# Kernel tuning notes

Hardware: AMD Instinct MI355X
Metric: run time of the kernel (lower is better)

The kernel has to match this reference:

```python
import jax, jax.numpy as jnp
import numpy as np

VOCAB, POS_V, NER_V, DEPREL_V = 50000, 50, 10, 40
EMB, POS_D, NER_D, MEM = 300, 30, 30, 200
NUM_LAYERS = 2


def setup_inputs() -> dict:
    key = jax.random.key(0)
    ks = jax.random.split(key, 12)
    B, L = 32, 100
    adj = jax.random.randint(ks[0], (B, L, L), 0, DEPREL_V)
    words = jax.random.randint(ks[1], (B, L), 0, VOCAB)
    pos = jax.random.randint(ks[2], (B, L), 0, POS_V)
    ner = jax.random.randint(ks[3], (B, L), 0, NER_V)
    s = 0.02
    emb = jax.random.normal(ks[4], (VOCAB, EMB), jnp.float32) * s
    pos_emb = jax.random.normal(ks[5], (POS_V, POS_D), jnp.float32) * s
    ner_emb = jax.random.normal(ks[6], (NER_V, NER_D), jnp.float32) * s
    deprel_emb = jax.random.normal(ks[7], (DEPREL_V, MEM), jnp.float32) * s
    deprel_emb = deprel_emb.at[0].set(0.0)  # padding_idx=0
    in_dim = EMB + POS_D + NER_D
    Wp = jax.random.normal(ks[8], (MEM, in_dim), jnp.float32) * s
    bp = jnp.zeros((MEM,), jnp.float32)
    W0 = jax.random.normal(ks[9], (MEM, MEM), jnp.float32) * s
    b0 = jnp.zeros((MEM,), jnp.float32)
    W1 = jax.random.normal(ks[10], (MEM, MEM), jnp.float32) * s
    b1 = jnp.zeros((MEM,), jnp.float32)
    return {"adj": adj, "words": words, "pos": pos, "ner": ner,
            "emb": emb, "pos_emb": pos_emb, "ner_emb": ner_emb,
            "deprel_emb": deprel_emb, "Wp": Wp, "bp": bp,
            "W0": W0, "b0": b0, "W1": W1, "b1": b1}


def reference(adj, words, pos, ner, emb, pos_emb, ner_emb, deprel_emb,
              Wp, bp, W0, b0, W1, b1):
    # embedding lookups + concat  -> [B, L, in_dim]
    embs = jnp.concatenate([emb[words], pos_emb[pos], ner_emb[ner]], axis=-1)
    # preprocessor linear (diagonal_deprel branch)  -> [B, L, D]
    x = embs @ Wp.T + bp
    # per-edge relation embedding gather  -> [B, L, L, D]
    deprel_adj = deprel_emb[adj]
    adj_m = (adj != 0).astype(jnp.float32)            # [B, L, L]
    denom = adj_m.sum(2)[..., None] + 1.0             # [B, L, 1]
    mask = ((adj_m.sum(2) + adj_m.sum(1)) == 0)[..., None]  # [B, L, 1]
    for W, b in ((W0, b0), (W1, b1)):
        # diagonal deprel aggregation: (deprel_adj * x[:,None]) summed over neighbors
        Ax = jnp.einsum('blmd,bmd->bld', deprel_adj, x)
        AxW = (Ax @ W.T + b) + (x @ W.T + b)
        x = jax.nn.relu(AxW / denom)
    return x, mask
```

## Files before the change

kernel.cpp:

```cpp
#include <hip/hip_runtime.h>
#include <hip/hip_bf16.h>

#define BB 32
#define LL 100
#define DD 200
#define KIN 360
#define NP (BB*LL)
#define RNUM 40
#define LT 13
#define NT 8

__device__ __forceinline__ void fma4(float4& a, const float4& w, float s) {
    a.x = fmaf(w.x, s, a.x);
    a.y = fmaf(w.y, s, a.y);
    a.z = fmaf(w.z, s, a.z);
    a.w = fmaf(w.w, s, a.w);
}
__device__ __forceinline__ unsigned bf16rn(float f) {
    unsigned u = __float_as_uint(f);
    return (u + 0x7fffu + ((u >> 16) & 1u)) >> 16;
}
__device__ __forceinline__ unsigned pk2(float a, float b) {
    return bf16rn(a) | (bf16rn(b) << 16);
}
__device__ __forceinline__ float lo16(unsigned u) { return __uint_as_float(u << 16); }
__device__ __forceinline__ float hi16(unsigned u) { return __uint_as_float(u & 0xffff0000u); }

__global__ __launch_bounds__(256) void prep_transpose_kernel(
        const int* __restrict__ adj,
        const float* __restrict__ Wp, const float* __restrict__ W0, const float* __restrict__ W1,
        float* __restrict__ WpT, float* __restrict__ W0T, float* __restrict__ W1T,
        float* __restrict__ invd, float* __restrict__ mask_out) {
    int bid = blockIdx.x, tid = threadIdx.x;
    if (bid < 25) {
        int t = bid * 256 + tid;
        int half = t & 1;
        int pl = t >> 1;
        int b = pl / LL, l = pl % LL;
        const int4* row = (const int4*)(adj + (size_t)pl * LL);
        int q0 = half ? 13 : 0, q1 = half ? 25 : 13;
        int rc = 0;
        for (int i = q0; i < q1; ++i) {
            int4 a = row[i];
            rc += (a.x != 0) + (a.y != 0) + (a.z != 0) + (a.w != 0);
        }
        const int* base = adj + (size_t)b * LL * LL + l;
        int cc = 0;
        for (int m = half * 50; m < half * 50 + 50; ++m) cc += (base[(size_t)m * LL] != 0);
        rc += __shfl_xor(rc, 1);
        cc += __shfl_xor(cc, 1);
        if (!half) {
            invd[pl] = 1.0f / (float)(rc + 1);
            mask_out[pl] = (rc + cc == 0) ? 1.0f : 0.0f;
        }
    } else {
        int i = (bid - 25) * 256 + tid;
        if (i < 18000) {
            int k = i / 50, o = (i % 50) * 4;
            float4 v;
            v.x = Wp[(size_t)(o + 0) * KIN + k];
            v.y = Wp[(size_t)(o + 1) * KIN + k];
            v.z = Wp[(size_t)(o + 2) * KIN + k];
            v.w = Wp[(size_t)(o + 3) * KIN + k];
            ((float4*)WpT)[i] = v;
        } else if (i < 28000) {
            int q = i - 18000;
            int k = q / 50, o = (q % 50) * 4;
            float4 v;
            v.x = W0[(size_t)(o + 0) * DD + k];
            v.y = W0[(size_t)(o + 1) * DD + k];
            v.z = W0[(size_t)(o + 2) * DD + k];
            v.w = W0[(size_t)(o + 3) * DD + k];
            ((float4*)W0T)[q] = v;
        } else if (i < 38000) {
            int q = i - 28000;
            int k = q / 50, o = (q % 50) * 4;
            float4 v;
            v.x = W1[(size_t)(o + 0) * DD + k];
            v.y = W1[(size_t)(o + 1) * DD + k];
            v.z = W1[(size_t)(o + 2) * DD + k];
            v.w = W1[(size_t)(o + 3) * DD + k];
            ((float4*)W1T)[q] = v;
        }
    }
}

__global__ __launch_bounds__(512, 4) void embed_gemv_kernel(
        const int* __restrict__ words, const int* __restrict__ pos, const int* __restrict__ ner,
        const float* __restrict__ emb, const float* __restrict__ pose, const float* __restrict__ nere,
        const float* __restrict__ wpt, const float* __restrict__ bp,
        float* __restrict__ xA) {
    __shared__ float es[8 * KIN];
    __shared__ float4 red[8 * 8 * 50];
    int tid = threadIdx.x;
    int pbase = blockIdx.x * 8;

    float2* es2 = (float2*)es;
    for (int idx = tid; idx < 8 * 180; idx += 512) {
        int p = idx / 180, j2 = idx % 180;
        int gp = pbase + p;
        float2 v;
        if (j2 < 150)      v = ((const float2*)emb)[(size_t)words[gp] * 150 + j2];
        else if (j2 < 165) v = ((const float2*)pose)[pos[gp] * 15 + (j2 - 150)];
        else               v = ((const float2*)nere)[ner[gp] * 15 + (j2 - 165)];
        es2[idx] = v;
    }
    __syncthreads();

    int lane = tid & 63, w = tid >> 6;
    bool act = lane < 50;
    int oq = act ? lane : 49;
    int kq0 = (w < 5) ? 12 * w : 60 + 10 * (w - 5);
    int npair = (w < 5) ? 6 : 5;
    int kqlast = kq0 + 2 * npair - 1;
    const float4* wt4 = (const float4*)wpt;
    const float4* es4 = (const float4*)es;

    float4 a[8];
    #pragma unroll
    for (int p = 0; p < 8; ++p) a[p] = make_float4(0.f, 0.f, 0.f, 0.f);

    float4 wc[8], wn[8];
    #pragma unroll
    for (int q = 0; q < 2; ++q)
        #pragma unroll
        for (int j = 0; j < 4; ++j)
            wc[q * 4 + j] = wt4[(size_t)(4 * (kq0 + q) + j) * 50 + oq];

    for (int pr = 0; pr < npair; ++pr) {
        int nb = kq0 + 2 * pr + 2;
        int nbA = nb <= kqlast ? nb : kq0;
        int nbB = nb + 1 <= kqlast ? nb + 1 : kq0;
        #pragma unroll
        for (int j = 0; j < 4; ++j) wn[j]     = wt4[(size_t)(4 * nbA + j) * 50 + oq];
        #pragma unroll
        for (int j = 0; j < 4; ++j) wn[4 + j] = wt4[(size_t)(4 * nbB + j) * 50 + oq];
        #pragma unroll
        for (int q = 0; q < 2; ++q) {
            int kq = kq0 + 2 * pr + q;
            #pragma unroll
            for (int p = 0; p < 8; ++p) {
                float4 s = es4[p * 90 + kq];
                fma4(a[p], wc[q * 4 + 0], s.x); fma4(a[p], wc[q * 4 + 1], s.y);
                fma4(a[p], wc[q * 4 + 2], s.z); fma4(a[p], wc[q * 4 + 3], s.w);
            }
        }
        #pragma unroll
        for (int j = 0; j < 8; ++j) wc[j] = wn[j];
    }

    if (act) {
        #pragma unroll
        for (int p = 0; p < 8; ++p) red[w * 400 + p * 50 + oq] = a[p];
    }
    __syncthreads();
    for (int t = tid; t < 400; t += 512) {
        int oq2 = t % 50;
        float4 v = ((const float4*)bp)[oq2];
        #pragma unroll
        for (int s = 0; s < 8; ++s) {
            float4 r = red[s * 400 + t];
            v.x += r.x; v.y += r.y; v.z += r.z; v.w += r.w;
        }
        ((float4*)xA)[(size_t)(pbase + t / 50) * 50 + oq2] = v;
    }
}

__global__ __launch_bounds__(1024, 4) void layer_kernel(
        const float* __restrict__ x, const int* __restrict__ adj,
        const float* __restrict__ deprel, const float* __restrict__ wt,
        const float* __restrict__ bias, const float* __restrict__ invd,
        float* __restrict__ out) {
    __shared__ alignas(16) char smem[58912];
    uint2* deps_b = (uint2*)smem;
    unsigned* adjp = (unsigned*)(smem + 16000);
    float4* Sh = (float4*)(smem + 17312);
    float4* Sfin = (float4*)smem;

    int b = blockIdx.y, tile = blockIdx.x;
    int l0 = tile * LT;
    int lcnt = min(LT, LL - l0);
    int tid = threadIdx.x;
    const float4* x4 = (const float4*)x;

    for (int i = tid; i < RNUM * 50; i += 1024) {
        float4 v = ((const float4*)deprel)[i];
        deps_b[i] = make_uint2(pk2(v.x, v.y), pk2(v.z, v.w));
    }
    for (int i = tid; i < lcnt * 25; i += 1024) {
        int li = i / 25, mg = i % 25;
        int4 a = ((const int4*)(adj + (size_t)(b * LL + l0 + li) * LL))[mg];
        adjp[i] = (unsigned)a.x | ((unsigned)a.y << 8) | ((unsigned)a.z << 16) | ((unsigned)a.w << 24);
    }
    __syncthreads();

    int lane = tid & 63, w = tid >> 6;
    int lg = w & 3, sq = w >> 2;
    bool act = lane < 50;
    int dq = lane;

    float4 acc[4];
    #pragma unroll
    for (int i = 0; i < 4; ++i) acc[i] = make_float4(0.f, 0.f, 0.f, 0.f);
    if (act) {
        int mg0 = (sq == 0) ? 0 : 1 + 6 * sq;
        int mg1 = mg0 + ((sq == 0) ? 7 : 6);
        float4 xc[4], xn[4];
        #pragma unroll
        for (int mm = 0; mm < 4; ++mm)
            xc[mm] = x4[(size_t)(b * LL + 4 * mg0 + mm) * 50 + dq];
        for (int mg = mg0; mg < mg1; ++mg) {
            int mgn = (mg + 1 < mg1) ? mg + 1 : mg;
            #pragma unroll
            for (int mm = 0; mm < 4; ++mm)
                xn[mm] = x4[(size_t)(b * LL + 4 * mgn + mm) * 50 + dq];
            unsigned ap[4];
            #pragma unroll
            for (int i = 0; i < 4; ++i) {
                int li = lg + 4 * i;
                ap[i] = (li < lcnt) ? adjp[li * 25 + mg] : 0u;
            }
            #pragma unroll
            for (int mm = 0; mm < 4; ++mm) {
                #pragma unroll
                for (int i = 0; i < 4; ++i) {
                    unsigned r = (ap[i] >> (8 * mm)) & 0xffu;
                    uint2 dv = deps_b[r * 50 + dq];
                    acc[i].x = fmaf(lo16(dv.x), xc[mm].x, acc[i].x);
                    acc[i].y = fmaf(hi16(dv.x), xc[mm].y, acc[i].y);
                    acc[i].z = fmaf(lo16(dv.y), xc[mm].z, acc[i].z);
                    acc[i].w = fmaf(hi16(dv.y), xc[mm].w, acc[i].w);
                }
            }
            #pragma unroll
            for (int mm = 0; mm < 4; ++mm) xc[mm] = xn[mm];
        }
        #pragma unroll
        for (int i = 0; i < 4; ++i) {
            int li = lg + 4 * i;
            if (li < lcnt) Sh[sq * 650 + li * 50 + dq] = acc[i];
        }
    }
    __syncthreads();

    for (int t2 = tid; t2 < 650; t2 += 1024) {
        int li = t2 / 50;
        if (li < lcnt) {
            float4 s0 = Sh[t2], s1 = Sh[650 + t2], s2 = Sh[1300 + t2], s3 = Sh[1950 + t2];
            float4 xr = x4[(size_t)(b * LL + l0 + li) * 50 + (t2 % 50)];
            float4 s;
            s.x = s0.x + s1.x + s2.x + s3.x + xr.x;
            s.y = s0.y + s1.y + s2.y + s3.y + xr.y;
            s.z = s0.z + s1.z + s2.z + s3.z + xr.z;
            s.w = s0.w + s1.w + s2.w + s3.w + xr.w;
            Sfin[t2] = s;
        }
    }
    __syncthreads();

    const float4* wt4 = (const float4*)wt;
    int oq = act ? lane : 49;
    int kq0 = (sq < 2) ? 13 * sq : 26 + 12 * (sq - 2);
    int kcnt = (sq < 2) ? 13 : 12;
    int npair = kcnt >> 1;
    int kqlast = kq0 + kcnt - 1;
    float4 ba[4];
    #pragma unroll
    for (int i = 0; i < 4; ++i) ba[i] = make_float4(0.f, 0.f, 0.f, 0.f);

    float4 wc[8], wn[8];
    #pragma unroll
    for (int q = 0; q < 2; ++q)
        #pragma unroll
        for (int j = 0; j < 4; ++j)
            wc[q * 4 + j] = wt4[(size_t)(4 * (kq0 + q) + j) * 50 + oq];

    int lic[4];
    #pragma unroll
    for (int i = 0; i < 4; ++i) {
        int li = lg + 4 * i;
        lic[i] = li < lcnt ? li : lcnt - 1;
    }

    for (int pr = 0; pr < npair; ++pr) {
        int nb = kq0 + 2 * pr + 2;
        int nbA = nb <= kqlast ? nb : kq0;
        int nbB = nb + 1 <= kqlast ? nb + 1 : kq0;
        #pragma unroll
        for (int j = 0; j < 4; ++j) wn[j]     = wt4[(size_t)(4 * nbA + j) * 50 + oq];
        #pragma unroll
        for (int j = 0; j < 4; ++j) wn[4 + j] = wt4[(size_t)(4 * nbB + j) * 50 + oq];
        #pragma unroll
        for (int q = 0; q < 2; ++q) {
            int kq = kq0 + 2 * pr + q;
            #pragma unroll
            for (int i = 0; i < 4; ++i) {
                float4 s = Sfin[lic[i] * 50 + kq];
                fma4(ba[i], wc[q * 4 + 0], s.x); fma4(ba[i], wc[q * 4 + 1], s.y);
                fma4(ba[i], wc[q * 4 + 2], s.z); fma4(ba[i], wc[q * 4 + 3], s.w);
            }
        }
        #pragma unroll
        for (int j = 0; j < 8; ++j) wc[j] = wn[j];
    }
    if (kcnt & 1) {
        #pragma unroll
        for (int i = 0; i < 4; ++i) {
            float4 s = Sfin[lic[i] * 50 + kqlast];
            fma4(ba[i], wc[0], s.x); fma4(ba[i], wc[1], s.y);
            fma4(ba[i], wc[2], s.z); fma4(ba[i], wc[3], s.w);
        }
    }

    if (act) {
        #pragma unroll
        for (int i = 0; i < 4; ++i) {
            int li = lg + 4 * i;
            if (li < lcnt) Sh[sq * 650 + li * 50 + oq] = ba[i];
        }
    }
    __syncthreads();

    for (int t2 = tid; t2 < 650; t2 += 1024) {
        int li = t2 / 50, oq2 = t2 % 50;
        if (li < lcnt) {
            float4 v0 = Sh[t2], v1 = Sh[650 + t2], v2 = Sh[1300 + t2], v3 = Sh[1950 + t2];
            float4 bb = ((const float4*)bias)[oq2];
            int p = b * LL + l0 + li;
            float sc = invd[p];
            float4 v;
            v.x = fmaxf((v0.x + v1.x + v2.x + v3.x + 2.f * bb.x) * sc, 0.f);
            v.y = fmaxf((v0.y + v1.y + v2.y + v3.y + 2.f * bb.y) * sc, 0.f);
            v.z = fmaxf((v0.z + v1.z + v2.z + v3.z + 2.f * bb.z) * sc, 0.f);
            v.w = fmaxf((v0.w + v1.w + v2.w + v3.w + 2.f * bb.w) * sc, 0.f);
            ((float4*)out)[(size_t)p * 50 + oq2] = v;
        }
    }
}

extern "C" void kernel_launch(void* const* d_in, const int* in_sizes, int n_in,
                              void* d_out, int out_size, void* d_ws, size_t ws_size,
                              hipStream_t stream) {
    const int*   adj   = (const int*)d_in[0];
    const int*   words = (const int*)d_in[1];
    const int*   pos   = (const int*)d_in[2];
    const int*   ner   = (const int*)d_in[3];
    const float* emb   = (const float*)d_in[4];
    const float* pose  = (const float*)d_in[5];
    const float* nere  = (const float*)d_in[6];
    const float* dep   = (const float*)d_in[7];
    const float* Wp    = (const float*)d_in[8];
    const float* bp    = (const float*)d_in[9];
    const float* W0    = (const float*)d_in[10];
    const float* b0    = (const float*)d_in[11];
    const float* W1    = (const float*)d_in[12];
    const float* b1    = (const float*)d_in[13];
    float* out = (float*)d_out;
    float* ws  = (float*)d_ws;

    float* xA   = ws;
    float* xB   = ws + 640000;
    float* WpT  = ws + 1280000;
    float* W0T  = ws + 1352000;
    float* W1T  = ws + 1392000;
    float* invd = ws + 1432000;

    prep_transpose_kernel<<<25 + 149, 256, 0, stream>>>(adj, Wp, W0, W1, WpT, W0T, W1T,
                                                        invd, out + (size_t)NP * DD);
    embed_gemv_kernel<<<NP / 8, 512, 0, stream>>>(words, pos, ner, emb, pose, nere,
                                                  WpT, bp, xA);
    layer_kernel<<<dim3(NT, BB), 1024, 0, stream>>>(xA, adj, dep, W0T, b0, invd, xB);
    layer_kernel<<<dim3(NT, BB), 1024, 0, stream>>>(xB, adj, dep, W1T, b1, invd, out);
}
```

Measured before the change: 69.80 us.

## Fuse adjacency stats and W0/W1 transpose into embedding GEMV launch

Splits out a small kernel that transposes only Wp, then merges the adjacency degree/mask computation and the W0/W1 transposes into the embedding GEMV launch as extra blocks. Degree counting now stages each batch's adjacency in LDS and counts rows and columns from there, instead of doing strided global column reads. The GEMV reduction is halved to four partial slots through a two-step LDS accumulate, which shrinks shared memory. Launch count stays the same, but the prep work now overlaps with the GEMV. The small Wp transpose kernel still serializes ahead of the GEMV.

```diff
diff --git a/kernel.cpp b/kernel.cpp
--- a/kernel.cpp
+++ b/kernel.cpp
@@ -5,7 +5,7 @@
 #define LL 100
 #define DD 200
 #define KIN 360
-#define NP (BB*LL)
+#define NP 3200
 #define RNUM 40
 #define LT 13
 #define NT 8
@@ -26,54 +26,43 @@
 __device__ __forceinline__ float lo16(unsigned u) { return __uint_as_float(u << 16); }
 __device__ __forceinline__ float hi16(unsigned u) { return __uint_as_float(u & 0xffff0000u); }
 
-__global__ __launch_bounds__(256) void prep_transpose_kernel(
+__global__ __launch_bounds__(512) void wpt_kernel(const float* __restrict__ Wp,
+                                                  float* __restrict__ WpT) {
+    int t = blockIdx.x * 512 + threadIdx.x;
+    if (t < 18000) {
+        int k = t / 50, o = (t % 50) * 4;
+        float4 v;
+        v.x = Wp[(size_t)(o + 0) * KIN + k];
+        v.y = Wp[(size_t)(o + 1) * KIN + k];
+        v.z = Wp[(size_t)(o + 2) * KIN + k];
+        v.w = Wp[(size_t)(o + 3) * KIN + k];
+        ((float4*)WpT)[t] = v;
+    }
+}
+
+__global__ __launch_bounds__(512, 4) void embed_prep_kernel(
+        const int* __restrict__ words, const int* __restrict__ pos, const int* __restrict__ ner,
+        const float* __restrict__ emb, const float* __restrict__ pose, const float* __restrict__ nere,
+        const float* __restrict__ wpt, const float* __restrict__ bp,
         const int* __restrict__ adj,
-        const float* __restrict__ Wp, const float* __restrict__ W0, const float* __restrict__ W1,
-        float* __restrict__ WpT, float* __restrict__ W0T, float* __restrict__ W1T,
-        float* __restrict__ invd, float* __restrict__ mask_out) {
+        const float* __restrict__ W0, const float* __restrict__ W1,
+        float* __restrict__ W0T, float* __restrict__ W1T,
+        float* __restrict__ xA, float* __restrict__ invd, float* __restrict__ mask_out) {
+    __shared__ alignas(16) char smem[40960];
     int bid = blockIdx.x, tid = threadIdx.x;
-    if (bid < 25) {
-        int t = bid * 256 + tid;
-        int half = t & 1;
-        int pl = t >> 1;
-        int b = pl / LL, l = pl % LL;
-        const int4* row = (const int4*)(adj + (size_t)pl * LL);
-        int q0 = half ? 13 : 0, q1 = half ? 25 : 13;
-        int rc = 0;
-        for (int i = q0; i < q1; ++i) {
-            int4 a = row[i];
-            rc += (a.x != 0) + (a.y != 0) + (a.z != 0) + (a.w != 0);
-        }
-        const int* base = adj + (size_t)b * LL * LL + l;
-        int cc = 0;
-        for (int m = half * 50; m < half * 50 + 50; ++m) cc += (base[(size_t)m * LL] != 0);
-        rc += __shfl_xor(rc, 1);
-        cc += __shfl_xor(cc, 1);
-        if (!half) {
-            invd[pl] = 1.0f / (float)(rc + 1);
-            mask_out[pl] = (rc + cc == 0) ? 1.0f : 0.0f;
-        }
-    } else {
-        int i = (bid - 25) * 256 + tid;
-        if (i < 18000) {
+
+    if (bid >= 432) {
+        int i = (bid - 432) * 512 + tid;
+        if (i < 10000) {
             int k = i / 50, o = (i % 50) * 4;
-            float4 v;
-            v.x = Wp[(size_t)(o + 0) * KIN + k];
-            v.y = Wp[(size_t)(o + 1) * KIN + k];
-            v.z = Wp[(size_t)(o + 2) * KIN + k];
-            v.w = Wp[(size_t)(o + 3) * KIN + k];
-            ((float4*)WpT)[i] = v;
-        } else if (i < 28000) {
-            int q = i - 18000;
-            int k = q / 50, o = (q % 50) * 4;
             float4 v;
             v.x = W0[(size_t)(o + 0) * DD + k];
             v.y = W0[(size_t)(o + 1) * DD + k];
             v.z = W0[(size_t)(o + 2) * DD + k];
             v.w = W0[(size_t)(o + 3) * DD + k];
-            ((float4*)W0T)[q] = v;
-        } else if (i < 38000) {
-            int q = i - 28000;
+            ((float4*)W0T)[i] = v;
+        } else if (i < 20000) {
+            int q = i - 10000;
             int k = q / 50, o = (q % 50) * 4;
             float4 v;
             v.x = W1[(size_t)(o + 0) * DD + k];
@@ -82,18 +71,40 @@
             v.w = W1[(size_t)(o + 3) * DD + k];
             ((float4*)W1T)[q] = v;
         }
-    }
-}
-
-__global__ __launch_bounds__(512, 4) void embed_gemv_kernel(
-        const int* __restrict__ words, const int* __restrict__ pos, const int* __restrict__ ner,
-        const float* __restrict__ emb, const float* __restrict__ pose, const float* __restrict__ nere,
-        const float* __restrict__ wpt, const float* __restrict__ bp,
-        float* __restrict__ xA) {
-    __shared__ float es[8 * KIN];
-    __shared__ float4 red[8 * 8 * 50];
-    int tid = threadIdx.x;
-    int pbase = blockIdx.x * 8;
+        return;
+    }
+
+    if (bid >= 400) {
+        int bb = bid - 400;
+        int* a_lds = (int*)smem;
+        int* rcc = (int*)(smem + 40000);
+        const int4* src = (const int4*)(adj + (size_t)bb * (LL * LL));
+        for (int i = tid; i < 2500; i += 512) ((int4*)a_lds)[i] = src[i];
+        __syncthreads();
+        if (tid < 200) {
+            int l = tid % 100;
+            int c = 0;
+            if (tid < 100) {
+                #pragma unroll 4
+                for (int m = 0; m < 100; ++m) c += (a_lds[l * 100 + m] != 0);
+            } else {
+                #pragma unroll 4
+                for (int m = 0; m < 100; ++m) c += (a_lds[m * 100 + l] != 0);
+            }
+            rcc[tid] = c;
+        }
+        __syncthreads();
+        if (tid < 100) {
+            int rc = rcc[tid], cc = rcc[100 + tid];
+            invd[bb * 100 + tid] = 1.0f / (float)(rc + 1);
+            mask_out[bb * 100 + tid] = (rc + cc == 0) ? 1.0f : 0.0f;
+        }
+        return;
+    }
+
+    float* es = (float*)smem;
+    float4* red = (float4*)(smem + 11520);
+    int pbase = bid * 8;
 
     float2* es2 = (float2*)es;
     for (int idx = tid; idx < 8 * 180; idx += 512) {
@@ -149,16 +160,25 @@
         for (int j = 0; j < 8; ++j) wc[j] = wn[j];
     }
 
-    if (act) {
-        #pragma unroll
-        for (int p = 0; p < 8; ++p) red[w * 400 + p * 50 + oq] = a[p];
+    if (w >= 4 && act) {
+        #pragma unroll
+        for (int p = 0; p < 8; ++p) red[(w - 4) * 400 + p * 50 + oq] = a[p];
+    }
+    __syncthreads();
+    if (w < 4 && act) {
+        #pragma unroll
+        for (int p = 0; p < 8; ++p) {
+            float4 r = red[w * 400 + p * 50 + oq];
+            r.x += a[p].x; r.y += a[p].y; r.z += a[p].z; r.w += a[p].w;
+            red[w * 400 + p * 50 + oq] = r;
+        }
     }
     __syncthreads();
     for (int t = tid; t < 400; t += 512) {
         int oq2 = t % 50;
         float4 v = ((const float4*)bp)[oq2];
         #pragma unroll
-        for (int s = 0; s < 8; ++s) {
+        for (int s = 0; s < 4; ++s) {
             float4 r = red[s * 400 + t];
             v.x += r.x; v.y += r.y; v.z += r.z; v.w += r.w;
         }
@@ -365,10 +385,10 @@
     float* W1T  = ws + 1392000;
     float* invd = ws + 1432000;
 
-    prep_transpose_kernel<<<25 + 149, 256, 0, stream>>>(adj, Wp, W0, W1, WpT, W0T, W1T,
-                                                        invd, out + (size_t)NP * DD);
-    embed_gemv_kernel<<<NP / 8, 512, 0, stream>>>(words, pos, ner, emb, pose, nere,
-                                                  WpT, bp, xA);
+    wpt_kernel<<<36, 512, 0, stream>>>(Wp, WpT);
+    embed_prep_kernel<<<472, 512, 0, stream>>>(words, pos, ner, emb, pose, nere,
+                                               WpT, bp, adj, W0, W1, W0T, W1T,
+                                               xA, invd, out + (size_t)NP * DD);
     layer_kernel<<<dim3(NT, BB), 1024, 0, stream>>>(xA, adj, dep, W0T, b0, invd, xB);
     layer_kernel<<<dim3(NT, BB), 1024, 0, stream>>>(xB, adj, dep, W1T, b1, invd, out);
 }
```

Result: faster. 62.24 us (-10.8%).
